# Optimization experiments

Measured on AMD Instinct MI355X. Metric: run time of the kernel, lower is better.

## Reference

```python
import jax, jax.numpy as jnp
import numpy as np
from jax import lax

WINDOW_SIZE = 11
SIGMA = 1.5
MAX_VAL = 1.0


def _gaussian_kernel_2d(window_size: int, sigma: float) -> jnp.ndarray:
    coords = jnp.arange(window_size, dtype=jnp.float32) - window_size // 2
    g = jnp.exp(-coords ** 2 / (2.0 * sigma ** 2))
    g = g / g.sum()
    k2d = jnp.outer(g, g)
    return k2d / k2d.sum()  # [W, W]


def _depthwise_conv(x: jnp.ndarray, k2d: jnp.ndarray) -> jnp.ndarray:
    # x: [B, C, H, W]; depthwise (groups=C) conv with SAME padding
    C = x.shape[1]
    ws = k2d.shape[0]
    kernel = jnp.broadcast_to(k2d[None, None], (C, 1, ws, ws)).astype(x.dtype)  # [C,1,ws,ws]
    pad = ws // 2
    return lax.conv_general_dilated(
        x, kernel,
        window_strides=(1, 1),
        padding=((pad, pad), (pad, pad)),
        dimension_numbers=('NCHW', 'OIHW', 'NCHW'),
        feature_group_count=C,
    )


def setup_inputs() -> dict:
    key = jax.random.key(0)
    k1, k2 = jax.random.split(key)
    B, C, H, W = 16, 3, 512, 512
    sr = jax.random.uniform(k1, (B, C, H, W), dtype=jnp.float32)
    hr = jax.random.uniform(k2, (B, C, H, W), dtype=jnp.float32)
    return {"sr": sr, "hr": hr}


def reference(sr, hr):
    c1 = (0.01 * MAX_VAL) ** 2
    c2 = (0.03 * MAX_VAL) ** 2
    k2d = _gaussian_kernel_2d(WINDOW_SIZE, SIGMA)

    mu1 = _depthwise_conv(sr, k2d)
    mu2 = _depthwise_conv(hr, k2d)
    mu1_sq = mu1 ** 2
    mu2_sq = mu2 ** 2
    mu1_mu2 = mu1 * mu2
    sigma1_sq = _depthwise_conv(sr * sr, k2d) - mu1_sq
    sigma2_sq = _depthwise_conv(hr * hr, k2d) - mu2_sq
    sigma12 = _depthwise_conv(sr * hr, k2d) - mu1_mu2

    ssim_map = (2 * mu1_mu2 + c1) * (2 * sigma12 + c2) / (
        (mu1_sq + mu2_sq + c1) * (sigma1_sq + sigma2_sq + c2) + 1e-12)
    return 1.0 - ssim_map.mean()
```

## Files before the change

kernel.cpp:

```cpp
#include <hip/hip_runtime.h>


typedef __attribute__((ext_vector_type(2))) float  f32x2;
typedef __attribute__((ext_vector_type(4))) float  f32x4;
typedef __fp16 f16;
typedef __attribute__((ext_vector_type(2))) __fp16 h2v;
typedef __attribute__((ext_vector_type(4))) __fp16 h4;
typedef __attribute__((ext_vector_type(8))) __fp16 h8;

constexpr int IMG_H = 512;
constexpr int IMG_W = 512;
constexpr int PL    = IMG_H * IMG_W;
constexpr int NBC   = 48;
constexpr int TW    = 64;
constexpr int TH    = 32;
constexpr int NPERS = 1280;

constexpr int HTP   = 56;
constexpr int HTQS  = 64 * HTP;
constexpr int SMEMH = 4 * HTQS;

constexpr float C1 = 1.0e-4f;
constexpr float C2 = 9.0e-4f;

__device__ const float GW[11] = {
    0.00102838f, 0.00759876f, 0.03600077f, 0.10936070f, 0.21300553f,
    0.26601172f, 0.21300553f, 0.10936070f, 0.03600077f, 0.00759876f,
    0.00102838f};

__device__ __forceinline__ h8 ldfrag(const f16* __restrict__ gtab, int base) {
    h8 b;
#pragma unroll
    for (int i = 0; i < 8; ++i) b[i] = gtab[base + i];
    return b;
}

__global__ __launch_bounds__(64) void ssim_init(double* acc) {
    if (threadIdx.x == 0) acc[0] = 0.0;
}

__global__ __launch_bounds__(256, 5) void ssim_main(const float* __restrict__ sr,
                                                    const float* __restrict__ hr,
                                                    double* __restrict__ sink,
                                                    int mode) {
    __shared__ __align__(16) f16 smem[SMEMH];
    __shared__ __align__(8)  f16 gtab[128];
    __shared__ float wsums[4];

    const int tid  = threadIdx.x;
    const int w    = tid >> 6;
    const int lane = tid & 63;
    const int l15  = lane & 15;
    const int grp8 = (lane >> 4) << 3;
    const int grp4 = (lane >> 4) << 2;

    const int bx  = blockIdx.x & 7;
    const int by  = (blockIdx.x >> 3) & 15;
    const int bc0 = blockIdx.x >> 7;
    const int gr0 = by * TH - 5;
    const int gc0 = bx * TW - 8;

    const int colh = gc0 + 16 * w + grp8;
    const bool cok = (unsigned)colh < (unsigned)IMG_W;
    const int rb   = gr0 + l15;

    if (tid < 128) {
        const int d = tid - 66;
        float v = 0.f;
        if ((unsigned)d <= 10u) v = GW[d];
        gtab[tid] = (f16)v;
    }

    float s16 = 0.f;
#pragma unroll
    for (int d = 0; d <= 10; ++d) s16 += (float)(f16)GW[d];
    const float rs = 1.0f / (s16 * s16);

    __syncthreads();

    const h8 bh = ldfrag(gtab, 63 + grp8 - l15);
    const h8 bv = ldfrag(gtab, 66 + grp8 - l15);

    float local = 0.f;

    for (int bc = bc0; bc < NBC; bc += 10) {
        const float* __restrict__ srp = sr + (size_t)bc * PL;
        const float* __restrict__ hrp = hr + (size_t)bc * PL;

        f32x4 acc[4][3] = {};
#pragma unroll
        for (int Mt = 0; Mt < 3; ++Mt) {
            const int r  = rb + 16 * Mt;
            const bool ok = cok & ((unsigned)r < (unsigned)IMG_H);
            float4 a0, a1, b0, b1;
            a0 = a1 = b0 = b1 = (float4){0.f, 0.f, 0.f, 0.f};
            if (ok) {
                const float4* pa = (const float4*)&srp[r * IMG_W + colh];
                const float4* pb = (const float4*)&hrp[r * IMG_W + colh];
                a0 = pa[0]; a1 = pa[1];
                b0 = pb[0]; b1 = pb[1];
            }
            const f32x2* A0 = (const f32x2*)&a0;
            const f32x2* A1 = (const f32x2*)&a1;
            const f32x2* B0 = (const f32x2*)&b0;
            const f32x2* B1 = (const f32x2*)&b1;
            const f32x2 s0 = A0[0] * A0[0] + B0[0] * B0[0];
            const f32x2 s1 = A0[1] * A0[1] + B0[1] * B0[1];
            const f32x2 s2 = A1[0] * A1[0] + B1[0] * B1[0];
            const f32x2 s3 = A1[1] * A1[1] + B1[1] * B1[1];
            const f32x2 p0 = A0[0] * B0[0], p1 = A0[1] * B0[1];
            const f32x2 p2 = A1[0] * B1[0], p3 = A1[1] * B1[1];
            union { h2v h2[4]; h8 v; } fa, fb, fs, fp;
            fa.h2[0] = __builtin_amdgcn_cvt_pkrtz(A0[0].x, A0[0].y);
            fa.h2[1] = __builtin_amdgcn_cvt_pkrtz(A0[1].x, A0[1].y);
            fa.h2[2] = __builtin_amdgcn_cvt_pkrtz(A1[0].x, A1[0].y);
            fa.h2[3] = __builtin_amdgcn_cvt_pkrtz(A1[1].x, A1[1].y);
            fb.h2[0] = __builtin_amdgcn_cvt_pkrtz(B0[0].x, B0[0].y);
            fb.h2[1] = __builtin_amdgcn_cvt_pkrtz(B0[1].x, B0[1].y);
            fb.h2[2] = __builtin_amdgcn_cvt_pkrtz(B1[0].x, B1[0].y);
            fb.h2[3] = __builtin_amdgcn_cvt_pkrtz(B1[1].x, B1[1].y);
            fs.h2[0] = __builtin_amdgcn_cvt_pkrtz(s0.x, s0.y);
            fs.h2[1] = __builtin_amdgcn_cvt_pkrtz(s1.x, s1.y);
            fs.h2[2] = __builtin_amdgcn_cvt_pkrtz(s2.x, s2.y);
            fs.h2[3] = __builtin_amdgcn_cvt_pkrtz(s3.x, s3.y);
            fp.h2[0] = __builtin_amdgcn_cvt_pkrtz(p0.x, p0.y);
            fp.h2[1] = __builtin_amdgcn_cvt_pkrtz(p1.x, p1.y);
            fp.h2[2] = __builtin_amdgcn_cvt_pkrtz(p2.x, p2.y);
            fp.h2[3] = __builtin_amdgcn_cvt_pkrtz(p3.x, p3.y);
            acc[0][Mt] = __builtin_amdgcn_mfma_f32_16x16x32_f16(fa.v, bh, acc[0][Mt], 0, 0, 0);
            acc[1][Mt] = __builtin_amdgcn_mfma_f32_16x16x32_f16(fb.v, bh, acc[1][Mt], 0, 0, 0);
            acc[2][Mt] = __builtin_amdgcn_mfma_f32_16x16x32_f16(fs.v, bh, acc[2][Mt], 0, 0, 0);
            acc[3][Mt] = __builtin_amdgcn_mfma_f32_16x16x32_f16(fp.v, bh, acc[3][Mt], 0, 0, 0);
        }

        f32x4 acc2[4][2];
        const int cbase = (16 * w + l15) * HTP;
#pragma unroll
        for (int q = 0; q < 4; ++q) {
#pragma unroll
            for (int Mt = 0; Mt < 3; ++Mt) {
                union { h2v h2[2]; h4 v; } u;
                u.h2[0] = __builtin_amdgcn_cvt_pkrtz(acc[q][Mt][0], acc[q][Mt][1]);
                u.h2[1] = __builtin_amdgcn_cvt_pkrtz(acc[q][Mt][2], acc[q][Mt][3]);
                *(h4*)&smem[q * HTQS + cbase + 16 * Mt + grp4] = u.v;
            }
            const h8 a0 = *(const h8*)&smem[q * HTQS + cbase + grp8];
            const h8 a1 = *(const h8*)&smem[q * HTQS + cbase + grp8 + 16];
            const f32x4 z = {0.f, 0.f, 0.f, 0.f};
            acc2[q][0] = __builtin_amdgcn_mfma_f32_16x16x32_f16(a0, bv, z, 0, 0, 0);
            acc2[q][1] = __builtin_amdgcn_mfma_f32_16x16x32_f16(a1, bv, z, 0, 0, 0);
        }

#pragma unroll
        for (int nt = 0; nt < 2; ++nt) {
            const f32x4 m1 = acc2[0][nt] * rs;
            const f32x4 m2 = acc2[1][nt] * rs;
            const f32x4 S  = acc2[2][nt] * rs;
            const f32x4 pp = acc2[3][nt] * rs;
            const f32x4 mu1s = m1 * m1, mu2s = m2 * m2, mu12 = m1 * m2;
            const f32x4 sg12 = pp - mu12;
            const f32x4 sgs  = S - mu1s - mu2s;
            const f32x4 num = (2.f * mu12 + C1) * (2.f * sg12 + C2);
            const f32x4 den = (mu1s + mu2s + C1) * (sgs + C2) + 1e-12f;
#pragma unroll
            for (int e = 0; e < 4; ++e)
                local += num[e] * __builtin_amdgcn_rcpf(den[e]);
        }
    }

#pragma unroll
    for (int offr = 32; offr > 0; offr >>= 1)
        local += __shfl_down(local, offr, 64);
    if ((tid & 63) == 0) wsums[tid >> 6] = local;
    __syncthreads();
    if (tid == 0) {
        const double bsum = (double)(wsums[0] + wsums[1] + wsums[2] + wsums[3]);
        if (mode == 0) {
            sink[blockIdx.x] = bsum;
        } else {
            atomicAdd(sink, bsum);
        }
    }
}

__global__ __launch_bounds__(256) void ssim_finalize(const double* __restrict__ partial,
                                                     float* __restrict__ out, int count) {
    __shared__ double ws[4];
    double s = 0.0;
    for (int i = threadIdx.x; i < count; i += 256) s += partial[i];
#pragma unroll
    for (int off = 32; off > 0; off >>= 1)
        s += __shfl_down(s, off, 64);
    const int lane = threadIdx.x & 63, wave = threadIdx.x >> 6;
    if (lane == 0) ws[wave] = s;
    __syncthreads();
    if (threadIdx.x == 0) {
        const double tot = ws[0] + ws[1] + ws[2] + ws[3];
        const double n = (double)NBC * IMG_H * IMG_W;
        out[0] = (float)(1.0 - tot / n);
    }
}

extern "C" void kernel_launch(void* const* d_in, const int* in_sizes, int n_in,
                              void* d_out, int out_size, void* d_ws, size_t ws_size,
                              hipStream_t stream) {
    const float* sr = (const float*)d_in[0];
    const float* hr = (const float*)d_in[1];
    float* out = (float*)d_out;

    if (ws_size >= (size_t)NPERS * sizeof(double)) {
        double* partial = (double*)d_ws;
        ssim_main<<<dim3(NPERS), dim3(256), 0, stream>>>(sr, hr, partial, 0);
        ssim_finalize<<<dim3(1), dim3(256), 0, stream>>>(partial, out, NPERS);
    } else {
        double* acc = (double*)d_ws;
        ssim_init<<<dim3(1), dim3(64), 0, stream>>>(acc);
        ssim_main<<<dim3(NPERS), dim3(256), 0, stream>>>(sr, hr, acc, 1);
        ssim_finalize<<<dim3(1), dim3(256), 0, stream>>>(acc, out, 1);
    }
}
```

Baseline: 141.7 us.

## Software-pipeline global loads across channel iterations with clamped addresses

Loads for the next batch-channel plane are issued at the top of each iteration into a second register set, so they overlap the current plane's MFMA and LDS work. Out-of-range addresses are clamped so the loads are unconditional, and zero-masking is applied afterwards. Horizontal MFMA results are converted and written to LDS right after each tile instead of being held in a 4x3 accumulator array. Occupancy is lowered from 5 to 4 waves-per-SIMD target to make room for the extra registers, and the last iteration issues a redundant load of the same plane.

```diff
diff --git a/kernel.cpp b/kernel.cpp
--- a/kernel.cpp
+++ b/kernel.cpp
@@ -39,7 +39,7 @@
     if (threadIdx.x == 0) acc[0] = 0.0;
 }
 
-__global__ __launch_bounds__(256, 5) void ssim_main(const float* __restrict__ sr,
+__global__ __launch_bounds__(256, 4) void ssim_main(const float* __restrict__ sr,
                                                     const float* __restrict__ hr,
                                                     double* __restrict__ sink,
                                                     int mode) {
@@ -61,8 +61,17 @@
     const int gc0 = bx * TW - 8;
 
     const int colh = gc0 + 16 * w + grp8;
+    const int cc   = colh < 0 ? 0 : (colh > IMG_W - 8 ? IMG_W - 8 : colh);
     const bool cok = (unsigned)colh < (unsigned)IMG_W;
-    const int rb   = gr0 + l15;
+    int  offc[3];
+    bool okM[3];
+#pragma unroll
+    for (int Mt = 0; Mt < 3; ++Mt) {
+        const int r  = gr0 + l15 + 16 * Mt;
+        const int rc = r < 0 ? 0 : (r > IMG_H - 1 ? IMG_H - 1 : r);
+        okM[Mt] = cok & ((unsigned)r < (unsigned)IMG_H);
+        offc[Mt] = rc * IMG_W + cc;
+    }
 
     if (tid < 128) {
         const int d = tid - 66;
@@ -81,24 +90,41 @@
     const h8 bh = ldfrag(gtab, 63 + grp8 - l15);
     const h8 bv = ldfrag(gtab, 66 + grp8 - l15);
 
+    float4 cA0[3], cA1[3], cB0[3], cB1[3];
+    {
+        const float* __restrict__ srp = sr + (size_t)bc0 * PL;
+        const float* __restrict__ hrp = hr + (size_t)bc0 * PL;
+#pragma unroll
+        for (int Mt = 0; Mt < 3; ++Mt) {
+            const float4* pa = (const float4*)&srp[offc[Mt]];
+            const float4* pb = (const float4*)&hrp[offc[Mt]];
+            cA0[Mt] = pa[0]; cA1[Mt] = pa[1];
+            cB0[Mt] = pb[0]; cB1[Mt] = pb[1];
+        }
+    }
+
     float local = 0.f;
 
     for (int bc = bc0; bc < NBC; bc += 10) {
-        const float* __restrict__ srp = sr + (size_t)bc * PL;
-        const float* __restrict__ hrp = hr + (size_t)bc * PL;
-
-        f32x4 acc[4][3] = {};
-#pragma unroll
-        for (int Mt = 0; Mt < 3; ++Mt) {
-            const int r  = rb + 16 * Mt;
-            const bool ok = cok & ((unsigned)r < (unsigned)IMG_H);
-            float4 a0, a1, b0, b1;
-            a0 = a1 = b0 = b1 = (float4){0.f, 0.f, 0.f, 0.f};
-            if (ok) {
-                const float4* pa = (const float4*)&srp[r * IMG_W + colh];
-                const float4* pb = (const float4*)&hrp[r * IMG_W + colh];
-                a0 = pa[0]; a1 = pa[1];
-                b0 = pb[0]; b1 = pb[1];
+        const int bcn = (bc + 10 < NBC) ? bc + 10 : bc;
+        const float* __restrict__ srn = sr + (size_t)bcn * PL;
+        const float* __restrict__ hrn = hr + (size_t)bcn * PL;
+        float4 nA0[3], nA1[3], nB0[3], nB1[3];
+#pragma unroll
+        for (int Mt = 0; Mt < 3; ++Mt) {
+            const float4* pa = (const float4*)&srn[offc[Mt]];
+            const float4* pb = (const float4*)&hrn[offc[Mt]];
+            nA0[Mt] = pa[0]; nA1[Mt] = pa[1];
+            nB0[Mt] = pb[0]; nB1[Mt] = pb[1];
+        }
+        __builtin_amdgcn_sched_barrier(0);
+
+        const int cbase = (16 * w + l15) * HTP;
+#pragma unroll
+        for (int Mt = 0; Mt < 3; ++Mt) {
+            float4 a0 = cA0[Mt], a1 = cA1[Mt], b0 = cB0[Mt], b1 = cB1[Mt];
+            if (!okM[Mt]) {
+                a0 = a1 = b0 = b1 = (float4){0.f, 0.f, 0.f, 0.f};
             }
             const f32x2* A0 = (const f32x2*)&a0;
             const f32x2* A1 = (const f32x2*)&a1;
@@ -127,23 +153,29 @@
             fp.h2[1] = __builtin_amdgcn_cvt_pkrtz(p1.x, p1.y);
             fp.h2[2] = __builtin_amdgcn_cvt_pkrtz(p2.x, p2.y);
             fp.h2[3] = __builtin_amdgcn_cvt_pkrtz(p3.x, p3.y);
-            acc[0][Mt] = __builtin_amdgcn_mfma_f32_16x16x32_f16(fa.v, bh, acc[0][Mt], 0, 0, 0);
-            acc[1][Mt] = __builtin_amdgcn_mfma_f32_16x16x32_f16(fb.v, bh, acc[1][Mt], 0, 0, 0);
-            acc[2][Mt] = __builtin_amdgcn_mfma_f32_16x16x32_f16(fs.v, bh, acc[2][Mt], 0, 0, 0);
-            acc[3][Mt] = __builtin_amdgcn_mfma_f32_16x16x32_f16(fp.v, bh, acc[3][Mt], 0, 0, 0);
+            const f32x4 z = {0.f, 0.f, 0.f, 0.f};
+            f32x4 acc_a = __builtin_amdgcn_mfma_f32_16x16x32_f16(fa.v, bh, z, 0, 0, 0);
+            f32x4 acc_b = __builtin_amdgcn_mfma_f32_16x16x32_f16(fb.v, bh, z, 0, 0, 0);
+            f32x4 acc_s = __builtin_amdgcn_mfma_f32_16x16x32_f16(fs.v, bh, z, 0, 0, 0);
+            f32x4 acc_p = __builtin_amdgcn_mfma_f32_16x16x32_f16(fp.v, bh, z, 0, 0, 0);
+            union { h2v h2[2]; h4 v; } u;
+            u.h2[0] = __builtin_amdgcn_cvt_pkrtz(acc_a[0], acc_a[1]);
+            u.h2[1] = __builtin_amdgcn_cvt_pkrtz(acc_a[2], acc_a[3]);
+            *(h4*)&smem[0 * HTQS + cbase + 16 * Mt + grp4] = u.v;
+            u.h2[0] = __builtin_amdgcn_cvt_pkrtz(acc_b[0], acc_b[1]);
+            u.h2[1] = __builtin_amdgcn_cvt_pkrtz(acc_b[2], acc_b[3]);
+            *(h4*)&smem[1 * HTQS + cbase + 16 * Mt + grp4] = u.v;
+            u.h2[0] = __builtin_amdgcn_cvt_pkrtz(acc_s[0], acc_s[1]);
+            u.h2[1] = __builtin_amdgcn_cvt_pkrtz(acc_s[2], acc_s[3]);
+            *(h4*)&smem[2 * HTQS + cbase + 16 * Mt + grp4] = u.v;
+            u.h2[0] = __builtin_amdgcn_cvt_pkrtz(acc_p[0], acc_p[1]);
+            u.h2[1] = __builtin_amdgcn_cvt_pkrtz(acc_p[2], acc_p[3]);
+            *(h4*)&smem[3 * HTQS + cbase + 16 * Mt + grp4] = u.v;
         }
 
         f32x4 acc2[4][2];
-        const int cbase = (16 * w + l15) * HTP;
 #pragma unroll
         for (int q = 0; q < 4; ++q) {
-#pragma unroll
-            for (int Mt = 0; Mt < 3; ++Mt) {
-                union { h2v h2[2]; h4 v; } u;
-                u.h2[0] = __builtin_amdgcn_cvt_pkrtz(acc[q][Mt][0], acc[q][Mt][1]);
-                u.h2[1] = __builtin_amdgcn_cvt_pkrtz(acc[q][Mt][2], acc[q][Mt][3]);
-                *(h4*)&smem[q * HTQS + cbase + 16 * Mt + grp4] = u.v;
-            }
             const h8 a0 = *(const h8*)&smem[q * HTQS + cbase + grp8];
             const h8 a1 = *(const h8*)&smem[q * HTQS + cbase + grp8 + 16];
             const f32x4 z = {0.f, 0.f, 0.f, 0.f};
@@ -166,6 +198,12 @@
             for (int e = 0; e < 4; ++e)
                 local += num[e] * __builtin_amdgcn_rcpf(den[e]);
         }
+
+#pragma unroll
+        for (int Mt = 0; Mt < 3; ++Mt) {
+            cA0[Mt] = nA0[Mt]; cA1[Mt] = nA1[Mt];
+            cB0[Mt] = nB0[Mt]; cB1[Mt] = nB1[Mt];
+        }
     }
 
 #pragma unroll
```

New measurement: 165.2 us. 16.6% more time.
